# Kernel tuning notes

Hardware: AMD Instinct MI355X
Metric: run time of the kernel (lower is better)

Reference implementation:

```python
import jax, jax.numpy as jnp
import numpy as np

B, C, H, W = 2, 512, 48, 48
HEADS = 8          # head_dim = C // HEADS = 64
GROUPS = 32        # min(32, ceil(512/4)) = 32
EPS = 1e-5


def setup_inputs() -> dict:
    key = jax.random.key(0)
    ks = jax.random.split(key, 5)
    return {
        "x": jax.random.normal(ks[0], (B, C, H, W), jnp.float32),
        "gn_w": jnp.ones((C,), jnp.float32),
        "gn_b": jnp.zeros((C,), jnp.float32),
        # 1x1 convs stored as [out, in] matrices
        "qkv_w": jax.random.normal(ks[1], (3 * C, C), jnp.float32) / np.float32(np.sqrt(C)),
        "qkv_b": jax.random.normal(ks[2], (3 * C,), jnp.float32) * 0.01,
        "proj_w": jax.random.normal(ks[3], (C, C), jnp.float32) / np.float32(np.sqrt(C)),
        "proj_b": jax.random.normal(ks[4], (C,), jnp.float32) * 0.01,
    }


def _group_norm(x, w, b):
    b_, c_, h_, w_ = x.shape
    xg = x.reshape(b_, GROUPS, c_ // GROUPS, h_, w_)
    mean = xg.mean(axis=(2, 3, 4), keepdims=True)
    var = xg.var(axis=(2, 3, 4), keepdims=True)  # biased, matches F.group_norm
    xn = ((xg - mean) * jax.lax.rsqrt(var + EPS)).reshape(b_, c_, h_, w_)
    return xn * w[None, :, None, None] + b[None, :, None, None]


def reference(x, gn_w, gn_b, qkv_w, qkv_b, proj_w, proj_b):
    bx, cx, hx, wx = x.shape
    d = cx // HEADS
    n = hx * wx
    xn = _group_norm(x, gn_w, gn_b)
    # qkv 1x1 conv -> [B, 3C, H, W]
    y = jnp.einsum('oc,bchw->bohw', qkv_w, xn) + qkv_b[None, :, None, None]
    # torch: y.reshape(B*heads, d, 3, N).unbind(2)  (channel layout: head, chan, qkv)
    qkv = y.reshape(bx * HEADS, d, 3, n)
    q, k, v = qkv[:, :, 0, :], qkv[:, :, 1, :], qkv[:, :, 2, :]
    scale = np.float32(1.0 / np.sqrt(d))
    # AttentionOp: fp32 QK^T + softmax over keys (axis=2)
    w_attn = jax.nn.softmax(jnp.einsum('ncq,nck->nqk', q, k * scale), axis=2)
    a = jnp.einsum('nqk,nck->ncq', w_attn, v).reshape(bx, cx, hx, wx)
    out = jnp.einsum('oc,bchw->bohw', proj_w, a) + proj_b[None, :, None, None]
    return out + x
```

## Files before the change

### kernel.cpp

```cpp
#include <hip/hip_runtime.h>

typedef __bf16 bf16;
typedef __bf16 bf16x8 __attribute__((ext_vector_type(8)));
typedef __bf16 bf16x4 __attribute__((ext_vector_type(4)));
typedef float f32x4 __attribute__((ext_vector_type(4)));

#define B_ 2
#define C_ 512
#define HW_ 2304
#define GROUPS_ 32
#define CPG_ 16
#define EPS_ 1e-5f
#define THR_ 8.0f
#define LOG2E_ 1.44269504f
#define EXP2(x) __builtin_amdgcn_exp2f(x)

__device__ __forceinline__ void gload_lds16(const bf16* g, bf16* l) {
  __builtin_amdgcn_global_load_lds((const __attribute__((address_space(1))) void*)g,
                                   (__attribute__((address_space(3))) void*)l, 16, 0, 0);
}

__global__ __launch_bounds__(256) void pre_k(const float* __restrict__ x,
                                             const float* __restrict__ qkv_w,
                                             const float* __restrict__ qkv_b,
                                             const float* __restrict__ proj_w,
                                             float* __restrict__ ps,
                                             float* __restrict__ pss,
                                             bf16* __restrict__ wqk,
                                             bf16* __restrict__ wv,
                                             bf16* __restrict__ wp,
                                             float* __restrict__ bqk,
                                             float* __restrict__ bv) {
  int blk = blockIdx.x;
  if (blk < 512) {
    int bg = blk >> 3, seg = blk & 7;
    const int n4 = CPG_ * HW_ / 4 / 8;
    const float4* p = (const float4*)(x + (long)bg * CPG_ * HW_) + (long)seg * n4;
    float s = 0.f, ss = 0.f;
    for (int i = threadIdx.x; i < n4; i += 256) {
      float4 v = p[i];
      s += v.x + v.y + v.z + v.w;
      ss += v.x * v.x + v.y * v.y + v.z * v.z + v.w * v.w;
    }
#pragma unroll
    for (int d = 1; d < 64; d <<= 1) { s += __shfl_xor(s, d); ss += __shfl_xor(ss, d); }
    __shared__ float rs[4], rss[4];
    int wave = threadIdx.x >> 6, lane = threadIdx.x & 63;
    if (lane == 0) { rs[wave] = s; rss[wave] = ss; }
    __syncthreads();
    if (threadIdx.x == 0) {
      ps[blk] = rs[0] + rs[1] + rs[2] + rs[3];
      pss[blk] = rss[0] + rss[1] + rss[2] + rss[3];
    }
  } else {
    int idx = (blk - 512) * 256 + threadIdx.x;
    int r = idx >> 9, c = idx & 511;
    {
      int src = (r < 512) ? 3 * r : 3 * (r - 512) + 1;
      float sc = (r < 512) ? 0.125f * LOG2E_ : 1.0f;
      wqk[idx] = (bf16)(qkv_w[(long)src * 512 + c] * sc);
    }
    if (r < 512) {
      wv[idx] = (bf16)(qkv_w[(long)(3 * r + 2) * 512 + c]);
      wp[idx] = (bf16)(proj_w[idx]);
    }
    if (idx < 1024) {
      int src = (idx < 512) ? 3 * idx : 3 * (idx - 512) + 1;
      float sc = (idx < 512) ? 0.125f * LOG2E_ : 1.0f;
      bqk[idx] = qkv_b[src] * sc;
    }
    if (idx < 512) bv[idx] = qkv_b[3 * idx + 2];
  }
}

__global__ __launch_bounds__(256) void gn_apply_k(const float* __restrict__ x,
                                                  const float* __restrict__ gw,
                                                  const float* __restrict__ gb,
                                                  const float* __restrict__ ps,
                                                  const float* __restrict__ pss,
                                                  bf16* __restrict__ xnT) {
  int n0 = blockIdx.x * 64, c0 = blockIdx.y * 32, b = blockIdx.z;
  int nn = n0 + (threadIdx.x & 63);
  int cb = c0 + ((threadIdx.x >> 6) << 3);
  int gi = b * GROUPS_ + (cb >> 4);
  float s = 0.f, ss = 0.f;
#pragma unroll
  for (int k = 0; k < 8; ++k) { s += ps[gi * 8 + k]; ss += pss[gi * 8 + k]; }
  const float invN = 1.0f / (float)(CPG_ * HW_);
  float mu = s * invN;
  float var = ss * invN - mu * mu;
  float rstd = rsqrtf(var + EPS_);
  bf16x8 o;
#pragma unroll
  for (int j = 0; j < 8; ++j) {
    int c = cb + j;
    float sc = rstd * gw[c];
    float sh = gb[c] - mu * sc;
    float v = x[((long)b * C_ + c) * HW_ + nn];
    o[j] = (bf16)(v * sc + sh);
  }
  *(bf16x8*)&xnT[((long)b * HW_ + nn) * C_ + cb] = o;
}

template <int BIAS_MODE, bool RESID, typename OUT_T>
__global__ __launch_bounds__(256) void gemm_k(const bf16* __restrict__ A,
                                              const bf16* __restrict__ BT,
                                              const float* __restrict__ bias,
                                              const float* __restrict__ resid,
                                              OUT_T* __restrict__ Cc,
                                              int M, int N,
                                              long sA, long sBT, long sC) {
  constexpr int KK = 512;
  constexpr int NSTEP = KK >> 6;
  int b = blockIdx.z;
  A += sA * b;
  BT += sBT * b;
  Cc += sC * b;
  const float* R = RESID ? (resid + sC * b) : nullptr;
  int m0 = blockIdx.y * 64, n0 = blockIdx.x * 64;
  int tid = threadIdx.x, lane = tid & 63, wave = tid >> 6;
  int wm = (wave >> 1) << 5, wn = (wave & 1) << 5;
  int fr = lane & 15, g = lane >> 4;
  __shared__ __align__(16) bf16 As[3][64 * 64];
  __shared__ __align__(16) bf16 Bs[3][64 * 64];
  int sr = tid >> 3;
  int swz = (((tid & 7) + sr) & 7) << 3;
  const bf16* gA = A + (long)(m0 + sr) * KK + swz;
  const bf16* gB = BT + (long)(n0 + sr) * KK + swz;
  int o0 = ((g - fr) & 7) << 3;
  int o1 = ((4 + g - fr) & 7) << 3;
  f32x4 acc[2][2] = {};
  gload_lds16(gA, &As[0][tid * 8]);
  gload_lds16(gA + 32 * KK, &As[0][2048 + tid * 8]);
  gload_lds16(gB, &Bs[0][tid * 8]);
  gload_lds16(gB + 32 * KK, &Bs[0][2048 + tid * 8]);
  gload_lds16(gA + 64, &As[1][tid * 8]);
  gload_lds16(gA + 32 * KK + 64, &As[1][2048 + tid * 8]);
  gload_lds16(gB + 64, &Bs[1][tid * 8]);
  gload_lds16(gB + 32 * KK + 64, &Bs[1][2048 + tid * 8]);
  asm volatile("s_waitcnt vmcnt(4)" ::: "memory");
  __builtin_amdgcn_s_barrier();
#pragma unroll
  for (int t = 0; t < NSTEP; ++t) {
    const int cur = t % 3;
    if (t + 2 < NSTEP) {
      const int nb = (t + 2) % 3;
      int k0 = (t + 2) << 6;
      gload_lds16(gA + k0, &As[nb][tid * 8]);
      gload_lds16(gA + 32 * KK + k0, &As[nb][2048 + tid * 8]);
      gload_lds16(gB + k0, &Bs[nb][tid * 8]);
      gload_lds16(gB + 32 * KK + k0, &Bs[nb][2048 + tid * 8]);
    }
    bf16x8 a00 = *(bf16x8*)&As[cur][(wm + fr) * 64 + o0];
    bf16x8 a01 = *(bf16x8*)&As[cur][(wm + fr) * 64 + o1];
    bf16x8 a10 = *(bf16x8*)&As[cur][(wm + 16 + fr) * 64 + o0];
    bf16x8 a11 = *(bf16x8*)&As[cur][(wm + 16 + fr) * 64 + o1];
    bf16x8 b00 = *(bf16x8*)&Bs[cur][(wn + fr) * 64 + o0];
    bf16x8 b01 = *(bf16x8*)&Bs[cur][(wn + fr) * 64 + o1];
    bf16x8 b10 = *(bf16x8*)&Bs[cur][(wn + 16 + fr) * 64 + o0];
    bf16x8 b11 = *(bf16x8*)&Bs[cur][(wn + 16 + fr) * 64 + o1];
    acc[0][0] = __builtin_amdgcn_mfma_f32_16x16x32_bf16(a00, b00, acc[0][0], 0, 0, 0);
    acc[0][0] = __builtin_amdgcn_mfma_f32_16x16x32_bf16(a01, b01, acc[0][0], 0, 0, 0);
    acc[0][1] = __builtin_amdgcn_mfma_f32_16x16x32_bf16(a00, b10, acc[0][1], 0, 0, 0);
    acc[0][1] = __builtin_amdgcn_mfma_f32_16x16x32_bf16(a01, b11, acc[0][1], 0, 0, 0);
    acc[1][0] = __builtin_amdgcn_mfma_f32_16x16x32_bf16(a10, b00, acc[1][0], 0, 0, 0);
    acc[1][0] = __builtin_amdgcn_mfma_f32_16x16x32_bf16(a11, b01, acc[1][0], 0, 0, 0);
    acc[1][1] = __builtin_amdgcn_mfma_f32_16x16x32_bf16(a10, b10, acc[1][1], 0, 0, 0);
    acc[1][1] = __builtin_amdgcn_mfma_f32_16x16x32_bf16(a11, b11, acc[1][1], 0, 0, 0);
    if (t + 2 < NSTEP) {
      asm volatile("s_waitcnt vmcnt(4) lgkmcnt(0)" ::: "memory");
    } else if (t + 1 < NSTEP) {
      asm volatile("s_waitcnt vmcnt(0) lgkmcnt(0)" ::: "memory");
    }
    if (t + 1 < NSTEP) __builtin_amdgcn_s_barrier();
  }
  int rbase = (lane >> 4) << 2;
#pragma unroll
  for (int mi = 0; mi < 2; ++mi)
#pragma unroll
    for (int nj = 0; nj < 2; ++nj)
#pragma unroll
      for (int reg = 0; reg < 4; ++reg) {
        int row = m0 + wm + (mi << 4) + rbase + reg;
        int col = n0 + wn + (nj << 4) + fr;
        float v = acc[mi][nj][reg];
        if (BIAS_MODE == 1) v += bias[row];
        if (BIAS_MODE == 2) v += bias[col];
        if (RESID) v += R[(long)row * N + col];
        Cc[(long)row * N + col] = (OUT_T)v;
      }
}

template <int NS>
__global__ __launch_bounds__(512) void attn_k(const bf16* __restrict__ yT,
                                              const bf16* __restrict__ V,
                                              bf16* __restrict__ Op,
                                              float* __restrict__ Mp,
                                              float* __restrict__ Lp) {
  const int n = HW_;
  constexpr int NT = (HW_ / NS) / 64;
  int bh = blockIdx.y, b = bh >> 3, h = bh & 7;
  int split = blockIdx.z;
  int q0 = blockIdx.x * 128;
  int kbeg = split * (n / NS);
  int tid = threadIdx.x, lane = tid & 63, wave = tid >> 6;
  int fr = lane & 15, g = lane >> 4, kg = g << 3;
  const bf16* yTb = yT + (long)b * n * 1024;
  const bf16* Vb = V + ((long)b * C_ + h * 64) * n;
  const bf16* Kb = yTb + 512 + h * 64;

  int qrow = q0 + (wave << 4) + fr;
  const bf16* qp = yTb + (long)qrow * 1024 + h * 64;
  bf16x8 qf0 = *(const bf16x8*)(qp + kg);
  bf16x8 qf1 = *(const bf16x8*)(qp + 32 + kg);

  __shared__ __align__(16) bf16 Kt[2][64][64];
  __shared__ __align__(16) bf16 Vt[2][64][64];

  int o0 = ((g + fr) & 7) << 3;
  int o1 = ((4 + g + fr) & 7) << 3;

  float m_run = -1e30f, l_run = 0.f;
  f32x4 oacc[4] = {};

  int r0 = tid >> 3;
  int ck = tid & 7;
  int c0e = ck << 3;
  int pk = ((ck + r0) & 7) << 3;
  int vs = (c0e & 32) | ((c0e & 8) << 1) | ((c0e & 16) >> 2);
  int cv = vs >> 3, sub = vs & 7;
  int pv0 = (((cv + r0) & 7) << 3) + sub;
  int pv1 = (((cv + 1 + r0) & 7) << 3) + sub;

  const bf16* kptr = Kb + (long)(kbeg + r0) * 1024 + c0e;
  const bf16* vptr = Vb + (long)r0 * n + kbeg + c0e;
  uint4 rk = *(const uint4*)kptr;
  uint4 rv = *(const uint4*)vptr;
  *(uint4*)&Kt[0][r0][pk] = rk;
  *(uint2*)&Vt[0][r0][pv0] = make_uint2(rv.x, rv.y);
  *(uint2*)&Vt[0][r0][pv1] = make_uint2(rv.z, rv.w);
  kptr += 64 * 1024;
  vptr += 64;
  rk = *(const uint4*)kptr;
  rv = *(const uint4*)vptr;
  __syncthreads();

  for (int t = 0; t < NT; ++t) {
    int cur = t & 1;
    f32x4 s[4] = {};
    __builtin_amdgcn_s_setprio(1);
#pragma unroll
    for (int nj = 0; nj < 4; ++nj) {
      bf16x8 kf0 = *(bf16x8*)&Kt[cur][(nj << 4) + fr][o0];
      bf16x8 kf1 = *(bf16x8*)&Kt[cur][(nj << 4) + fr][o1];
      s[nj] = __builtin_amdgcn_mfma_f32_16x16x32_bf16(kf0, qf0, s[nj], 0, 0, 0);
      s[nj] = __builtin_amdgcn_mfma_f32_16x16x32_bf16(kf1, qf1, s[nj], 0, 0, 0);
    }
    __builtin_amdgcn_s_setprio(0);
    if (t + 1 < NT) {
      int nb = cur ^ 1;
      *(uint4*)&Kt[nb][r0][pk] = rk;
      *(uint2*)&Vt[nb][r0][pv0] = make_uint2(rv.x, rv.y);
      *(uint2*)&Vt[nb][r0][pv1] = make_uint2(rv.z, rv.w);
      if (t + 2 < NT) {
        kptr += 64 * 1024;
        vptr += 64;
        rk = *(const uint4*)kptr;
        rv = *(const uint4*)vptr;
      }
    }
    float pm = fmaxf(fmaxf(s[0][0], s[0][1]), fmaxf(s[0][2], s[0][3]));
#pragma unroll
    for (int nj = 1; nj < 4; ++nj)
      pm = fmaxf(pm, fmaxf(fmaxf(s[nj][0], s[nj][1]), fmaxf(s[nj][2], s[nj][3])));
    pm = fmaxf(pm, __shfl_xor(pm, 16));
    pm = fmaxf(pm, __shfl_xor(pm, 32));
    if (__any(pm > m_run + THR_)) {
      float mn = fmaxf(m_run, pm);
      float corr = EXP2(m_run - mn);
      m_run = mn;
      l_run *= corr;
#pragma unroll
      for (int dj = 0; dj < 4; ++dj)
#pragma unroll
        for (int r = 0; r < 4; ++r) oacc[dj][r] *= corr;
    }
    float ls = 0.f;
    bf16x8 pa0, pa1;
#pragma unroll
    for (int r = 0; r < 4; ++r) {
      float p0 = EXP2(s[0][r] - m_run);
      float p1 = EXP2(s[1][r] - m_run);
      float p2 = EXP2(s[2][r] - m_run);
      float p3 = EXP2(s[3][r] - m_run);
      ls += (p0 + p1) + (p2 + p3);
      pa0[r] = (bf16)p0;
      pa0[4 + r] = (bf16)p1;
      pa1[r] = (bf16)p2;
      pa1[4 + r] = (bf16)p3;
    }
    ls += __shfl_xor(ls, 16);
    ls += __shfl_xor(ls, 32);
    l_run += ls;
    __builtin_amdgcn_s_setprio(1);
#pragma unroll
    for (int dj = 0; dj < 4; ++dj) {
      bf16x8 vf0 = *(bf16x8*)&Vt[cur][(dj << 4) + fr][o0];
      bf16x8 vf1 = *(bf16x8*)&Vt[cur][(dj << 4) + fr][o1];
      oacc[dj] = __builtin_amdgcn_mfma_f32_16x16x32_bf16(vf0, pa0, oacc[dj], 0, 0, 0);
      oacc[dj] = __builtin_amdgcn_mfma_f32_16x16x32_bf16(vf1, pa1, oacc[dj], 0, 0, 0);
    }
    __builtin_amdgcn_s_setprio(0);
    __syncthreads();
  }
  long orow = (long)(split * 16 + bh) * n + q0 + (wave << 4) + fr;
#pragma unroll
  for (int dj = 0; dj < 4; ++dj) {
    bf16x4 ov = {(bf16)oacc[dj][0], (bf16)oacc[dj][1], (bf16)oacc[dj][2], (bf16)oacc[dj][3]};
    *(bf16x4*)&Op[orow * 64 + (dj << 4) + (g << 2)] = ov;
  }
  if (g == 0) {
    Mp[orow] = m_run;
    Lp[orow] = l_run;
  }
}

template <int NS>
__global__ __launch_bounds__(256) void attn_merge_k(const bf16* __restrict__ Op,
                                                    const float* __restrict__ Mp,
                                                    const float* __restrict__ Lp,
                                                    bf16* __restrict__ aT) {
  int bh = blockIdx.y, b = bh >> 3, h = bh & 7;
  int gi = blockIdx.x * 256 + threadIdx.x;
  int nrow = gi >> 3, dd8 = (gi & 7) << 3;
  long idx[NS];
  float mm = -1e30f;
#pragma unroll
  for (int s = 0; s < NS; ++s) {
    idx[s] = (long)(s * 16 + bh) * HW_ + nrow;
    mm = fmaxf(mm, Mp[idx[s]]);
  }
  float l = 0.f, w[NS];
#pragma unroll
  for (int s = 0; s < NS; ++s) {
    w[s] = EXP2(Mp[idx[s]] - mm);
    l += Lp[idx[s]] * w[s];
  }
  float invl = 1.f / l;
  float oaccf[8] = {};
#pragma unroll
  for (int s = 0; s < NS; ++s) {
    bf16x8 o = *(const bf16x8*)&Op[idx[s] * 64 + dd8];
    float ws = w[s] * invl;
#pragma unroll
    for (int j = 0; j < 8; ++j) oaccf[j] += (float)o[j] * ws;
  }
  bf16x8 o;
#pragma unroll
  for (int j = 0; j < 8; ++j) o[j] = (bf16)oaccf[j];
  *(bf16x8*)&aT[((long)b * HW_ + nrow) * C_ + h * 64 + dd8] = o;
}

extern "C" void kernel_launch(void* const* d_in, const int* in_sizes, int n_in,
                              void* d_out, int out_size, void* d_ws, size_t ws_size,
                              hipStream_t stream) {
  const float* x = (const float*)d_in[0];
  const float* gn_w = (const float*)d_in[1];
  const float* gn_b = (const float*)d_in[2];
  const float* qkv_w = (const float*)d_in[3];
  const float* qkv_b = (const float*)d_in[4];
  const float* proj_w = (const float*)d_in[5];
  const float* proj_b = (const float*)d_in[6];
  float* out = (float*)d_out;

  char* ws = (char*)d_ws;
  float* ps = (float*)ws;   ws += 2048;
  float* pss = (float*)ws;  ws += 2048;
  float* bqk = (float*)ws;  ws += 4096;
  float* bv = (float*)ws;   ws += 2048;
  bf16* wqk = (bf16*)ws;    ws += 1024l * 512 * 2;
  bf16* wv = (bf16*)ws;     ws += 512l * 512 * 2;
  bf16* wp = (bf16*)ws;     ws += 512l * 512 * 2;
  bf16* xnT = (bf16*)ws;    ws += 2l * HW_ * 512 * 2;
  bf16* yT = (bf16*)ws;     ws += 2l * HW_ * 1024 * 2;
  bf16* v = (bf16*)ws;      ws += 2l * 512 * HW_ * 2;
  bf16* aT = (bf16*)ws;     ws += 2l * HW_ * 512 * 2;
  bf16* Op = (bf16*)ws;
  size_t base_used = (size_t)(ws - (char*)d_ws);
  size_t need4 = base_used + 4ull * 16 * HW_ * 64 * 2 + 2ull * 4 * 16 * HW_ * 4;
  int NS = (ws_size >= need4) ? 4 : 2;
  ws += (size_t)NS * 16 * HW_ * 64 * 2;
  float* Mp = (float*)ws;   ws += (size_t)NS * 16 * HW_ * 4;
  float* Lp = (float*)ws;   ws += (size_t)NS * 16 * HW_ * 4;

  pre_k<<<2560, 256, 0, stream>>>(x, qkv_w, qkv_b, proj_w, ps, pss, wqk, wv, wp, bqk, bv);
  gn_apply_k<<<dim3(36, 16, 2), 256, 0, stream>>>(x, gn_w, gn_b, ps, pss, xnT);
  gemm_k<2, false, bf16><<<dim3(16, 36, 2), 256, 0, stream>>>(
      xnT, wqk, bqk, nullptr, yT, 2304, 1024, (long)HW_ * 512, 0, (long)HW_ * 1024);
  gemm_k<1, false, bf16><<<dim3(36, 8, 2), 256, 0, stream>>>(
      wv, xnT, bv, nullptr, v, 512, 2304, 0, (long)HW_ * 512, 512l * HW_);
  if (NS == 4) {
    attn_k<4><<<dim3(18, 16, 4), 512, 0, stream>>>(yT, v, Op, Mp, Lp);
    attn_merge_k<4><<<dim3(72, 16), 256, 0, stream>>>(Op, Mp, Lp, aT);
  } else {
    attn_k<2><<<dim3(18, 16, 2), 512, 0, stream>>>(yT, v, Op, Mp, Lp);
    attn_merge_k<2><<<dim3(72, 16), 256, 0, stream>>>(Op, Mp, Lp, aT);
  }
  gemm_k<1, true, float><<<dim3(36, 8, 2), 256, 0, stream>>>(
      wp, aT, proj_b, x, out, 512, 2304, 0, (long)HW_ * 512, 512l * HW_);
}
```

Measured before the change: 85.68 us.

## Switch attention to 32x32x16 MFMA with 32 queries per wave and fixed 2-way split

Rewrites the flash-attention kernel to use 32x32x16 bf16 MFMA instead of 16x16x32. Each of 4 waves (256 threads) now owns 32 query rows, with new LDS swizzles for K and V tiles. The kernel also drops the 4-way key split in favour of a fixed 2-way split, which halves the partial outputs the merge kernel reads. The larger MFMA tiles cut LDS fragment traffic and cross-lane shuffles per FLOP, at the cost of fewer blocks and waves for latency hiding and more accumulator registers per thread.

```diff
diff --git a/kernel.cpp b/kernel.cpp
--- a/kernel.cpp
+++ b/kernel.cpp
@@ -4,6 +4,7 @@
 typedef __bf16 bf16x8 __attribute__((ext_vector_type(8)));
 typedef __bf16 bf16x4 __attribute__((ext_vector_type(4)));
 typedef float f32x4 __attribute__((ext_vector_type(4)));
+typedef float f32x16 __attribute__((ext_vector_type(16)));
 
 #define B_ 2
 #define C_ 512
@@ -191,89 +192,99 @@
       }
 }
 
-template <int NS>
-__global__ __launch_bounds__(512) void attn_k(const bf16* __restrict__ yT,
+__global__ __launch_bounds__(256) void attn_k(const bf16* __restrict__ yT,
                                               const bf16* __restrict__ V,
                                               bf16* __restrict__ Op,
                                               float* __restrict__ Mp,
                                               float* __restrict__ Lp) {
   const int n = HW_;
+  constexpr int NS = 2;
   constexpr int NT = (HW_ / NS) / 64;
-  int bh = blockIdx.y, b = bh >> 3, h = bh & 7;
+  int bh = blockIdx.y, b = bh >> 3, head = bh & 7;
   int split = blockIdx.z;
   int q0 = blockIdx.x * 128;
   int kbeg = split * (n / NS);
   int tid = threadIdx.x, lane = tid & 63, wave = tid >> 6;
-  int fr = lane & 15, g = lane >> 4, kg = g << 3;
+  int ql = lane & 31, hi = lane >> 5;
   const bf16* yTb = yT + (long)b * n * 1024;
-  const bf16* Vb = V + ((long)b * C_ + h * 64) * n;
-  const bf16* Kb = yTb + 512 + h * 64;
-
-  int qrow = q0 + (wave << 4) + fr;
-  const bf16* qp = yTb + (long)qrow * 1024 + h * 64;
-  bf16x8 qf0 = *(const bf16x8*)(qp + kg);
-  bf16x8 qf1 = *(const bf16x8*)(qp + 32 + kg);
+  const bf16* Vb = V + ((long)b * C_ + head * 64) * n;
+  const bf16* Kb = yTb + 512 + head * 64;
+
+  int qrow = q0 + (wave << 5) + ql;
+  const bf16* qp = yTb + (long)qrow * 1024 + head * 64 + (hi << 3);
+  bf16x8 qf[4];
+#pragma unroll
+  for (int ds = 0; ds < 4; ++ds) qf[ds] = *(const bf16x8*)(qp + (ds << 4));
 
   __shared__ __align__(16) bf16 Kt[2][64][64];
   __shared__ __align__(16) bf16 Vt[2][64][64];
 
-  int o0 = ((g + fr) & 7) << 3;
-  int o1 = ((4 + g + fr) & 7) << 3;
+  int rotb = hi + (lane & 7);
 
   float m_run = -1e30f, l_run = 0.f;
-  f32x4 oacc[4] = {};
+  f32x16 oacc0 = {}, oacc1 = {};
 
   int r0 = tid >> 3;
   int ck = tid & 7;
   int c0e = ck << 3;
   int pk = ((ck + r0) & 7) << 3;
-  int vs = (c0e & 32) | ((c0e & 8) << 1) | ((c0e & 16) >> 2);
-  int cv = vs >> 3, sub = vs & 7;
-  int pv0 = (((cv + r0) & 7) << 3) + sub;
-  int pv1 = (((cv + 1 + r0) & 7) << 3) + sub;
+  int kl0 = (c0e & 48) | ((c0e & 8) >> 1);
+  int pv0 = ((((kl0 >> 3) + r0) & 7) << 3) | (kl0 & 7);
+  int pv1 = ((((kl0 >> 3) + 1 + r0) & 7) << 3) | (kl0 & 7);
 
   const bf16* kptr = Kb + (long)(kbeg + r0) * 1024 + c0e;
   const bf16* vptr = Vb + (long)r0 * n + kbeg + c0e;
-  uint4 rk = *(const uint4*)kptr;
-  uint4 rv = *(const uint4*)vptr;
-  *(uint4*)&Kt[0][r0][pk] = rk;
-  *(uint2*)&Vt[0][r0][pv0] = make_uint2(rv.x, rv.y);
-  *(uint2*)&Vt[0][r0][pv1] = make_uint2(rv.z, rv.w);
+  uint4 rk0 = *(const uint4*)kptr;
+  uint4 rk1 = *(const uint4*)(kptr + 32 * 1024);
+  uint4 rv0 = *(const uint4*)vptr;
+  uint4 rv1 = *(const uint4*)(vptr + 32 * n);
+  *(uint4*)&Kt[0][r0][pk] = rk0;
+  *(uint4*)&Kt[0][r0 + 32][pk] = rk1;
+  *(uint2*)&Vt[0][r0][pv0] = make_uint2(rv0.x, rv0.y);
+  *(uint2*)&Vt[0][r0][pv1] = make_uint2(rv0.z, rv0.w);
+  *(uint2*)&Vt[0][r0 + 32][pv0] = make_uint2(rv1.x, rv1.y);
+  *(uint2*)&Vt[0][r0 + 32][pv1] = make_uint2(rv1.z, rv1.w);
   kptr += 64 * 1024;
   vptr += 64;
-  rk = *(const uint4*)kptr;
-  rv = *(const uint4*)vptr;
+  rk0 = *(const uint4*)kptr;
+  rk1 = *(const uint4*)(kptr + 32 * 1024);
+  rv0 = *(const uint4*)vptr;
+  rv1 = *(const uint4*)(vptr + 32 * n);
   __syncthreads();
 
   for (int t = 0; t < NT; ++t) {
     int cur = t & 1;
-    f32x4 s[4] = {};
+    f32x16 s0 = {}, s1 = {};
     __builtin_amdgcn_s_setprio(1);
 #pragma unroll
-    for (int nj = 0; nj < 4; ++nj) {
-      bf16x8 kf0 = *(bf16x8*)&Kt[cur][(nj << 4) + fr][o0];
-      bf16x8 kf1 = *(bf16x8*)&Kt[cur][(nj << 4) + fr][o1];
-      s[nj] = __builtin_amdgcn_mfma_f32_16x16x32_bf16(kf0, qf0, s[nj], 0, 0, 0);
-      s[nj] = __builtin_amdgcn_mfma_f32_16x16x32_bf16(kf1, qf1, s[nj], 0, 0, 0);
+    for (int ds = 0; ds < 4; ++ds) {
+      int off = (((ds << 1) + rotb) & 7) << 3;
+      bf16x8 kf0 = *(bf16x8*)&Kt[cur][ql][off];
+      bf16x8 kf1 = *(bf16x8*)&Kt[cur][32 + ql][off];
+      s0 = __builtin_amdgcn_mfma_f32_32x32x16_bf16(kf0, qf[ds], s0, 0, 0, 0);
+      s1 = __builtin_amdgcn_mfma_f32_32x32x16_bf16(kf1, qf[ds], s1, 0, 0, 0);
     }
     __builtin_amdgcn_s_setprio(0);
     if (t + 1 < NT) {
       int nb = cur ^ 1;
-      *(uint4*)&Kt[nb][r0][pk] = rk;
-      *(uint2*)&Vt[nb][r0][pv0] = make_uint2(rv.x, rv.y);
-      *(uint2*)&Vt[nb][r0][pv1] = make_uint2(rv.z, rv.w);
+      *(uint4*)&Kt[nb][r0][pk] = rk0;
+      *(uint4*)&Kt[nb][r0 + 32][pk] = rk1;
+      *(uint2*)&Vt[nb][r0][pv0] = make_uint2(rv0.x, rv0.y);
+      *(uint2*)&Vt[nb][r0][pv1] = make_uint2(rv0.z, rv0.w);
+      *(uint2*)&Vt[nb][r0 + 32][pv0] = make_uint2(rv1.x, rv1.y);
+      *(uint2*)&Vt[nb][r0 + 32][pv1] = make_uint2(rv1.z, rv1.w);
       if (t + 2 < NT) {
         kptr += 64 * 1024;
         vptr += 64;
-        rk = *(const uint4*)kptr;
-        rv = *(const uint4*)vptr;
+        rk0 = *(const uint4*)kptr;
+        rk1 = *(const uint4*)(kptr + 32 * 1024);
+        rv0 = *(const uint4*)vptr;
+        rv1 = *(const uint4*)(vptr + 32 * n);
       }
     }
-    float pm = fmaxf(fmaxf(s[0][0], s[0][1]), fmaxf(s[0][2], s[0][3]));
-#pragma unroll
-    for (int nj = 1; nj < 4; ++nj)
-      pm = fmaxf(pm, fmaxf(fmaxf(s[nj][0], s[nj][1]), fmaxf(s[nj][2], s[nj][3])));
-    pm = fmaxf(pm, __shfl_xor(pm, 16));
+    float pm = fmaxf(s0[0], s1[0]);
+#pragma unroll
+    for (int r = 1; r < 16; ++r) pm = fmaxf(pm, fmaxf(s0[r], s1[r]));
     pm = fmaxf(pm, __shfl_xor(pm, 32));
     if (__any(pm > m_run + THR_)) {
       float mn = fmaxf(m_run, pm);
@@ -281,45 +292,45 @@
       m_run = mn;
       l_run *= corr;
 #pragma unroll
-      for (int dj = 0; dj < 4; ++dj)
-#pragma unroll
-        for (int r = 0; r < 4; ++r) oacc[dj][r] *= corr;
+      for (int r = 0; r < 16; ++r) { oacc0[r] *= corr; oacc1[r] *= corr; }
     }
     float ls = 0.f;
-    bf16x8 pa0, pa1;
-#pragma unroll
-    for (int r = 0; r < 4; ++r) {
-      float p0 = EXP2(s[0][r] - m_run);
-      float p1 = EXP2(s[1][r] - m_run);
-      float p2 = EXP2(s[2][r] - m_run);
-      float p3 = EXP2(s[3][r] - m_run);
-      ls += (p0 + p1) + (p2 + p3);
-      pa0[r] = (bf16)p0;
-      pa0[4 + r] = (bf16)p1;
-      pa1[r] = (bf16)p2;
-      pa1[4 + r] = (bf16)p3;
-    }
-    ls += __shfl_xor(ls, 16);
+    bf16x8 pa[2][2];
+#pragma unroll
+    for (int r = 0; r < 16; ++r) {
+      float p0 = EXP2(s0[r] - m_run);
+      float p1 = EXP2(s1[r] - m_run);
+      ls += p0 + p1;
+      pa[0][r >> 3][r & 7] = (bf16)p0;
+      pa[1][r >> 3][r & 7] = (bf16)p1;
+    }
     ls += __shfl_xor(ls, 32);
     l_run += ls;
     __builtin_amdgcn_s_setprio(1);
 #pragma unroll
-    for (int dj = 0; dj < 4; ++dj) {
-      bf16x8 vf0 = *(bf16x8*)&Vt[cur][(dj << 4) + fr][o0];
-      bf16x8 vf1 = *(bf16x8*)&Vt[cur][(dj << 4) + fr][o1];
-      oacc[dj] = __builtin_amdgcn_mfma_f32_16x16x32_bf16(vf0, pa0, oacc[dj], 0, 0, 0);
-      oacc[dj] = __builtin_amdgcn_mfma_f32_16x16x32_bf16(vf1, pa1, oacc[dj], 0, 0, 0);
-    }
+    for (int m = 0; m < 2; ++m)
+#pragma unroll
+      for (int sl = 0; sl < 2; ++sl) {
+        int off = (((m << 2) + (sl << 1) + rotb) & 7) << 3;
+        bf16x8 vf0 = *(bf16x8*)&Vt[cur][ql][off];
+        bf16x8 vf1 = *(bf16x8*)&Vt[cur][32 + ql][off];
+        oacc0 = __builtin_amdgcn_mfma_f32_32x32x16_bf16(vf0, pa[m][sl], oacc0, 0, 0, 0);
+        oacc1 = __builtin_amdgcn_mfma_f32_32x32x16_bf16(vf1, pa[m][sl], oacc1, 0, 0, 0);
+      }
     __builtin_amdgcn_s_setprio(0);
     __syncthreads();
   }
-  long orow = (long)(split * 16 + bh) * n + q0 + (wave << 4) + fr;
-#pragma unroll
-  for (int dj = 0; dj < 4; ++dj) {
-    bf16x4 ov = {(bf16)oacc[dj][0], (bf16)oacc[dj][1], (bf16)oacc[dj][2], (bf16)oacc[dj][3]};
-    *(bf16x4*)&Op[orow * 64 + (dj << 4) + (g << 2)] = ov;
-  }
-  if (g == 0) {
+  long orow = (long)(split * 16 + bh) * n + q0 + (wave << 5) + ql;
+#pragma unroll
+  for (int rg = 0; rg < 4; ++rg) {
+    bf16x4 ov0 = {(bf16)oacc0[rg * 4 + 0], (bf16)oacc0[rg * 4 + 1],
+                  (bf16)oacc0[rg * 4 + 2], (bf16)oacc0[rg * 4 + 3]};
+    bf16x4 ov1 = {(bf16)oacc1[rg * 4 + 0], (bf16)oacc1[rg * 4 + 1],
+                  (bf16)oacc1[rg * 4 + 2], (bf16)oacc1[rg * 4 + 3]};
+    *(bf16x4*)&Op[orow * 64 + (rg << 3) + (hi << 2)] = ov0;
+    *(bf16x4*)&Op[orow * 64 + 32 + (rg << 3) + (hi << 2)] = ov1;
+  }
+  if (hi == 0) {
     Mp[orow] = m_run;
     Lp[orow] = l_run;
   }
@@ -385,13 +396,9 @@
   bf16* yT = (bf16*)ws;     ws += 2l * HW_ * 1024 * 2;
   bf16* v = (bf16*)ws;      ws += 2l * 512 * HW_ * 2;
   bf16* aT = (bf16*)ws;     ws += 2l * HW_ * 512 * 2;
-  bf16* Op = (bf16*)ws;
-  size_t base_used = (size_t)(ws - (char*)d_ws);
-  size_t need4 = base_used + 4ull * 16 * HW_ * 64 * 2 + 2ull * 4 * 16 * HW_ * 4;
-  int NS = (ws_size >= need4) ? 4 : 2;
-  ws += (size_t)NS * 16 * HW_ * 64 * 2;
-  float* Mp = (float*)ws;   ws += (size_t)NS * 16 * HW_ * 4;
-  float* Lp = (float*)ws;   ws += (size_t)NS * 16 * HW_ * 4;
+  bf16* Op = (bf16*)ws;     ws += 2l * 16 * HW_ * 64 * 2;
+  float* Mp = (float*)ws;   ws += 2l * 16 * HW_ * 4;
+  float* Lp = (float*)ws;   ws += 2l * 16 * HW_ * 4;
 
   pre_k<<<2560, 256, 0, stream>>>(x, qkv_w, qkv_b, proj_w, ps, pss, wqk, wv, wp, bqk, bv);
   gn_apply_k<<<dim3(36, 16, 2), 256, 0, stream>>>(x, gn_w, gn_b, ps, pss, xnT);
@@ -399,13 +406,8 @@
       xnT, wqk, bqk, nullptr, yT, 2304, 1024, (long)HW_ * 512, 0, (long)HW_ * 1024);
   gemm_k<1, false, bf16><<<dim3(36, 8, 2), 256, 0, stream>>>(
       wv, xnT, bv, nullptr, v, 512, 2304, 0, (long)HW_ * 512, 512l * HW_);
-  if (NS == 4) {
-    attn_k<4><<<dim3(18, 16, 4), 512, 0, stream>>>(yT, v, Op, Mp, Lp);
-    attn_merge_k<4><<<dim3(72, 16), 256, 0, stream>>>(Op, Mp, Lp, aT);
-  } else {
-    attn_k<2><<<dim3(18, 16, 2), 512, 0, stream>>>(yT, v, Op, Mp, Lp);
-    attn_merge_k<2><<<dim3(72, 16), 256, 0, stream>>>(Op, Mp, Lp, aT);
-  }
+  attn_k<<<dim3(18, 16, 2), 256, 0, stream>>>(yT, v, Op, Mp, Lp);
+  attn_merge_k<2><<<dim3(72, 16), 256, 0, stream>>>(Op, Mp, Lp, aT);
   gemm_k<1, true, float><<<dim3(36, 8, 2), 256, 0, stream>>>(
       wp, aT, proj_b, x, out, 512, 2304, 0, (long)HW_ * 512, 512l * HW_);
 }
```

Measured after the change: 93.50 us. 1.09x slower.

## Give each attention wave two query groups and load K via direct-to-LDS

Applied to the files above, without the earlier changes.

The attention kernel drops from 512 to 256 threads per block, and each wave now handles two 16-row query groups. Each K/V fragment read from LDS is reused across twice as many MFMAs, halving LDS fragment reads per FLOP. K tiles are now loaded with global_load_lds, written straight to LDS with a swizzled source address, so they skip the register staging path. The trade-off is doubled accumulator and softmax state per thread, which adds register pressure, and fewer waves per block to hide latency.

```diff
diff --git a/kernel.cpp b/kernel.cpp
--- a/kernel.cpp
+++ b/kernel.cpp
@@ -192,136 +192,158 @@
 }
 
 template <int NS>
-__global__ __launch_bounds__(512) void attn_k(const bf16* __restrict__ yT,
-                                              const bf16* __restrict__ V,
-                                              bf16* __restrict__ Op,
-                                              float* __restrict__ Mp,
-                                              float* __restrict__ Lp) {
+__global__ __launch_bounds__(256, 4) void attn_k(const bf16* __restrict__ yT,
+                                                 const bf16* __restrict__ V,
+                                                 bf16* __restrict__ Op,
+                                                 float* __restrict__ Mp,
+                                                 float* __restrict__ Lp) {
   const int n = HW_;
   constexpr int NT = (HW_ / NS) / 64;
-  int bh = blockIdx.y, b = bh >> 3, h = bh & 7;
+  int bh = blockIdx.y, b = bh >> 3, head = bh & 7;
   int split = blockIdx.z;
   int q0 = blockIdx.x * 128;
   int kbeg = split * (n / NS);
   int tid = threadIdx.x, lane = tid & 63, wave = tid >> 6;
-  int fr = lane & 15, g = lane >> 4, kg = g << 3;
+  int fr = lane & 15, lg = lane >> 4, kg = lg << 3;
   const bf16* yTb = yT + (long)b * n * 1024;
-  const bf16* Vb = V + ((long)b * C_ + h * 64) * n;
-  const bf16* Kb = yTb + 512 + h * 64;
-
-  int qrow = q0 + (wave << 4) + fr;
-  const bf16* qp = yTb + (long)qrow * 1024 + h * 64;
-  bf16x8 qf0 = *(const bf16x8*)(qp + kg);
-  bf16x8 qf1 = *(const bf16x8*)(qp + 32 + kg);
+  const bf16* Vb = V + ((long)b * C_ + head * 64) * n;
+  const bf16* Kb = yTb + 512 + head * 64;
+
+  bf16x8 qf[2][2];
+#pragma unroll
+  for (int grp = 0; grp < 2; ++grp) {
+    const bf16* qp = yTb + (long)(q0 + grp * 64 + (wave << 4) + fr) * 1024 + head * 64;
+    qf[grp][0] = *(const bf16x8*)(qp + kg);
+    qf[grp][1] = *(const bf16x8*)(qp + 32 + kg);
+  }
 
   __shared__ __align__(16) bf16 Kt[2][64][64];
   __shared__ __align__(16) bf16 Vt[2][64][64];
 
-  int o0 = ((g + fr) & 7) << 3;
-  int o1 = ((4 + g + fr) & 7) << 3;
-
-  float m_run = -1e30f, l_run = 0.f;
-  f32x4 oacc[4] = {};
+  int ko0 = ((lg - fr) & 7) << 3;
+  int ko1 = ((4 + lg - fr) & 7) << 3;
+  int vo0 = ((lg + fr) & 7) << 3;
+  int vo1 = ((4 + lg + fr) & 7) << 3;
+
+  float m_run[2] = {-1e30f, -1e30f}, l_run[2] = {0.f, 0.f};
+  f32x4 oacc[2][4] = {};
 
   int r0 = tid >> 3;
   int ck = tid & 7;
   int c0e = ck << 3;
-  int pk = ((ck + r0) & 7) << 3;
+  int ksw = (((tid & 7) + r0) & 7) << 3;
+  const bf16* kSrc = Kb + (long)(kbeg + r0) * 1024 + ksw;
   int vs = (c0e & 32) | ((c0e & 8) << 1) | ((c0e & 16) >> 2);
   int cv = vs >> 3, sub = vs & 7;
   int pv0 = (((cv + r0) & 7) << 3) + sub;
   int pv1 = (((cv + 1 + r0) & 7) << 3) + sub;
 
-  const bf16* kptr = Kb + (long)(kbeg + r0) * 1024 + c0e;
   const bf16* vptr = Vb + (long)r0 * n + kbeg + c0e;
-  uint4 rk = *(const uint4*)kptr;
-  uint4 rv = *(const uint4*)vptr;
-  *(uint4*)&Kt[0][r0][pk] = rk;
-  *(uint2*)&Vt[0][r0][pv0] = make_uint2(rv.x, rv.y);
-  *(uint2*)&Vt[0][r0][pv1] = make_uint2(rv.z, rv.w);
-  kptr += 64 * 1024;
+  uint4 rv0 = *(const uint4*)vptr;
+  uint4 rv1 = *(const uint4*)(vptr + 32 * n);
+  gload_lds16(kSrc, &Kt[0][0][0] + tid * 8);
+  gload_lds16(kSrc + 32 * 1024, &Kt[0][32][0] + tid * 8);
+  *(uint2*)&Vt[0][r0][pv0] = make_uint2(rv0.x, rv0.y);
+  *(uint2*)&Vt[0][r0][pv1] = make_uint2(rv0.z, rv0.w);
+  *(uint2*)&Vt[0][r0 + 32][pv0] = make_uint2(rv1.x, rv1.y);
+  *(uint2*)&Vt[0][r0 + 32][pv1] = make_uint2(rv1.z, rv1.w);
   vptr += 64;
-  rk = *(const uint4*)kptr;
-  rv = *(const uint4*)vptr;
+  rv0 = *(const uint4*)vptr;
+  rv1 = *(const uint4*)(vptr + 32 * n);
   __syncthreads();
 
   for (int t = 0; t < NT; ++t) {
     int cur = t & 1;
-    f32x4 s[4] = {};
+    f32x4 s[2][4] = {};
     __builtin_amdgcn_s_setprio(1);
 #pragma unroll
     for (int nj = 0; nj < 4; ++nj) {
-      bf16x8 kf0 = *(bf16x8*)&Kt[cur][(nj << 4) + fr][o0];
-      bf16x8 kf1 = *(bf16x8*)&Kt[cur][(nj << 4) + fr][o1];
-      s[nj] = __builtin_amdgcn_mfma_f32_16x16x32_bf16(kf0, qf0, s[nj], 0, 0, 0);
-      s[nj] = __builtin_amdgcn_mfma_f32_16x16x32_bf16(kf1, qf1, s[nj], 0, 0, 0);
+      bf16x8 kf0 = *(bf16x8*)&Kt[cur][(nj << 4) + fr][ko0];
+      bf16x8 kf1 = *(bf16x8*)&Kt[cur][(nj << 4) + fr][ko1];
+      s[0][nj] = __builtin_amdgcn_mfma_f32_16x16x32_bf16(kf0, qf[0][0], s[0][nj], 0, 0, 0);
+      s[0][nj] = __builtin_amdgcn_mfma_f32_16x16x32_bf16(kf1, qf[0][1], s[0][nj], 0, 0, 0);
+      s[1][nj] = __builtin_amdgcn_mfma_f32_16x16x32_bf16(kf0, qf[1][0], s[1][nj], 0, 0, 0);
+      s[1][nj] = __builtin_amdgcn_mfma_f32_16x16x32_bf16(kf1, qf[1][1], s[1][nj], 0, 0, 0);
     }
     __builtin_amdgcn_s_setprio(0);
     if (t + 1 < NT) {
       int nb = cur ^ 1;
-      *(uint4*)&Kt[nb][r0][pk] = rk;
-      *(uint2*)&Vt[nb][r0][pv0] = make_uint2(rv.x, rv.y);
-      *(uint2*)&Vt[nb][r0][pv1] = make_uint2(rv.z, rv.w);
+      kSrc += 64 * 1024;
+      gload_lds16(kSrc, &Kt[nb][0][0] + tid * 8);
+      gload_lds16(kSrc + 32 * 1024, &Kt[nb][32][0] + tid * 8);
+      *(uint2*)&Vt[nb][r0][pv0] = make_uint2(rv0.x, rv0.y);
+      *(uint2*)&Vt[nb][r0][pv1] = make_uint2(rv0.z, rv0.w);
+      *(uint2*)&Vt[nb][r0 + 32][pv0] = make_uint2(rv1.x, rv1.y);
+      *(uint2*)&Vt[nb][r0 + 32][pv1] = make_uint2(rv1.z, rv1.w);
       if (t + 2 < NT) {
-        kptr += 64 * 1024;
         vptr += 64;
-        rk = *(const uint4*)kptr;
-        rv = *(const uint4*)vptr;
+        rv0 = *(const uint4*)vptr;
+        rv1 = *(const uint4*)(vptr + 32 * n);
       }
     }
-    float pm = fmaxf(fmaxf(s[0][0], s[0][1]), fmaxf(s[0][2], s[0][3]));
-#pragma unroll
-    for (int nj = 1; nj < 4; ++nj)
-      pm = fmaxf(pm, fmaxf(fmaxf(s[nj][0], s[nj][1]), fmaxf(s[nj][2], s[nj][3])));
-    pm = fmaxf(pm, __shfl_xor(pm, 16));
-    pm = fmaxf(pm, __shfl_xor(pm, 32));
-    if (__any(pm > m_run + THR_)) {
-      float mn = fmaxf(m_run, pm);
-      float corr = EXP2(m_run - mn);
-      m_run = mn;
-      l_run *= corr;
-#pragma unroll
-      for (int dj = 0; dj < 4; ++dj)
-#pragma unroll
-        for (int r = 0; r < 4; ++r) oacc[dj][r] *= corr;
-    }
-    float ls = 0.f;
-    bf16x8 pa0, pa1;
-#pragma unroll
-    for (int r = 0; r < 4; ++r) {
-      float p0 = EXP2(s[0][r] - m_run);
-      float p1 = EXP2(s[1][r] - m_run);
-      float p2 = EXP2(s[2][r] - m_run);
-      float p3 = EXP2(s[3][r] - m_run);
-      ls += (p0 + p1) + (p2 + p3);
-      pa0[r] = (bf16)p0;
-      pa0[4 + r] = (bf16)p1;
-      pa1[r] = (bf16)p2;
-      pa1[4 + r] = (bf16)p3;
-    }
-    ls += __shfl_xor(ls, 16);
-    ls += __shfl_xor(ls, 32);
-    l_run += ls;
+    bf16x8 pa[2][2];
+#pragma unroll
+    for (int grp = 0; grp < 2; ++grp) {
+      float pm = fmaxf(fmaxf(s[grp][0][0], s[grp][0][1]), fmaxf(s[grp][0][2], s[grp][0][3]));
+#pragma unroll
+      for (int nj = 1; nj < 4; ++nj)
+        pm = fmaxf(pm, fmaxf(fmaxf(s[grp][nj][0], s[grp][nj][1]),
+                             fmaxf(s[grp][nj][2], s[grp][nj][3])));
+      pm = fmaxf(pm, __shfl_xor(pm, 16));
+      pm = fmaxf(pm, __shfl_xor(pm, 32));
+      if (__any(pm > m_run[grp] + THR_)) {
+        float mn = fmaxf(m_run[grp], pm);
+        float corr = EXP2(m_run[grp] - mn);
+        m_run[grp] = mn;
+        l_run[grp] *= corr;
+#pragma unroll
+        for (int dj = 0; dj < 4; ++dj)
+#pragma unroll
+          for (int r = 0; r < 4; ++r) oacc[grp][dj][r] *= corr;
+      }
+      float ls = 0.f;
+#pragma unroll
+      for (int r = 0; r < 4; ++r) {
+        float p0 = EXP2(s[grp][0][r] - m_run[grp]);
+        float p1 = EXP2(s[grp][1][r] - m_run[grp]);
+        float p2 = EXP2(s[grp][2][r] - m_run[grp]);
+        float p3 = EXP2(s[grp][3][r] - m_run[grp]);
+        ls += (p0 + p1) + (p2 + p3);
+        pa[grp][0][r] = (bf16)p0;
+        pa[grp][0][4 + r] = (bf16)p1;
+        pa[grp][1][r] = (bf16)p2;
+        pa[grp][1][4 + r] = (bf16)p3;
+      }
+      ls += __shfl_xor(ls, 16);
+      ls += __shfl_xor(ls, 32);
+      l_run[grp] += ls;
+    }
     __builtin_amdgcn_s_setprio(1);
 #pragma unroll
     for (int dj = 0; dj < 4; ++dj) {
-      bf16x8 vf0 = *(bf16x8*)&Vt[cur][(dj << 4) + fr][o0];
-      bf16x8 vf1 = *(bf16x8*)&Vt[cur][(dj << 4) + fr][o1];
-      oacc[dj] = __builtin_amdgcn_mfma_f32_16x16x32_bf16(vf0, pa0, oacc[dj], 0, 0, 0);
-      oacc[dj] = __builtin_amdgcn_mfma_f32_16x16x32_bf16(vf1, pa1, oacc[dj], 0, 0, 0);
+      bf16x8 vf0 = *(bf16x8*)&Vt[cur][(dj << 4) + fr][vo0];
+      bf16x8 vf1 = *(bf16x8*)&Vt[cur][(dj << 4) + fr][vo1];
+      oacc[0][dj] = __builtin_amdgcn_mfma_f32_16x16x32_bf16(vf0, pa[0][0], oacc[0][dj], 0, 0, 0);
+      oacc[0][dj] = __builtin_amdgcn_mfma_f32_16x16x32_bf16(vf1, pa[0][1], oacc[0][dj], 0, 0, 0);
+      oacc[1][dj] = __builtin_amdgcn_mfma_f32_16x16x32_bf16(vf0, pa[1][0], oacc[1][dj], 0, 0, 0);
+      oacc[1][dj] = __builtin_amdgcn_mfma_f32_16x16x32_bf16(vf1, pa[1][1], oacc[1][dj], 0, 0, 0);
     }
     __builtin_amdgcn_s_setprio(0);
     __syncthreads();
   }
-  long orow = (long)(split * 16 + bh) * n + q0 + (wave << 4) + fr;
-#pragma unroll
-  for (int dj = 0; dj < 4; ++dj) {
-    bf16x4 ov = {(bf16)oacc[dj][0], (bf16)oacc[dj][1], (bf16)oacc[dj][2], (bf16)oacc[dj][3]};
-    *(bf16x4*)&Op[orow * 64 + (dj << 4) + (g << 2)] = ov;
-  }
-  if (g == 0) {
-    Mp[orow] = m_run;
-    Lp[orow] = l_run;
+#pragma unroll
+  for (int grp = 0; grp < 2; ++grp) {
+    long orow = (long)(split * 16 + bh) * n + q0 + grp * 64 + (wave << 4) + fr;
+#pragma unroll
+    for (int dj = 0; dj < 4; ++dj) {
+      bf16x4 ov = {(bf16)oacc[grp][dj][0], (bf16)oacc[grp][dj][1],
+                   (bf16)oacc[grp][dj][2], (bf16)oacc[grp][dj][3]};
+      *(bf16x4*)&Op[orow * 64 + (dj << 4) + (lg << 2)] = ov;
+    }
+    if (lg == 0) {
+      Mp[orow] = m_run[grp];
+      Lp[orow] = l_run[grp];
+    }
   }
 }
 
@@ -400,10 +422,10 @@
   gemm_k<1, false, bf16><<<dim3(36, 8, 2), 256, 0, stream>>>(
       wv, xnT, bv, nullptr, v, 512, 2304, 0, (long)HW_ * 512, 512l * HW_);
   if (NS == 4) {
-    attn_k<4><<<dim3(18, 16, 4), 512, 0, stream>>>(yT, v, Op, Mp, Lp);
+    attn_k<4><<<dim3(18, 16, 4), 256, 0, stream>>>(yT, v, Op, Mp, Lp);
     attn_merge_k<4><<<dim3(72, 16), 256, 0, stream>>>(Op, Mp, Lp, aT);
   } else {
-    attn_k<2><<<dim3(18, 16, 2), 512, 0, stream>>>(yT, v, Op, Mp, Lp);
+    attn_k<2><<<dim3(18, 16, 2), 256, 0, stream>>>(yT, v, Op, Mp, Lp);
     attn_merge_k<2><<<dim3(72, 16), 256, 0, stream>>>(Op, Mp, Lp, aT);
   }
   gemm_k<1, true, float><<<dim3(36, 8, 2), 256, 0, stream>>>(
```

After: 85.50 us. Within noise of the previous version (-0.2%).
